# Performance work log

Hardware: AMD Instinct MI355X
Metric: run time of the kernel (lower is better)

The kernel has to match this reference:

```python
import jax, jax.numpy as jnp
import numpy as np

EPS = 1e-6

def _layernorm(x, g, b):
    m = jnp.mean(x, axis=-1, keepdims=True)
    v = jnp.var(x, axis=-1, keepdims=True)
    return (x - m) / jnp.sqrt(v + EPS) * g + b

def setup_inputs() -> dict:
    key = jax.random.key(0)
    ks = jax.random.split(key, 12)
    B, L, D, H = 2, 1024, 1024, 16
    s = 0.02  # weight init scale
    return {
        "query": jax.random.normal(ks[0], (B, L, D), jnp.float32),
        "pos_bias": jax.random.normal(ks[1], (H, L, L), jnp.float32) * 0.1,
        "postag_bias": jax.random.normal(ks[2], (B, H, L, L), jnp.float32) * 0.1,
        "lex_mask": jax.random.normal(ks[3], (B, L), jnp.float32) * 0.1,
        "mask": jax.random.randint(ks[4], (B, L), 0, 2).astype(jnp.int32),
        "Wq": jax.random.normal(ks[5], (D, D), jnp.float32) * s,
        "bq": jnp.zeros((D,), jnp.float32),
        "Wk": jax.random.normal(ks[6], (D, D), jnp.float32) * s,
        "bk": jnp.zeros((D,), jnp.float32),
        "Wv": jax.random.normal(ks[7], (D, D), jnp.float32) * s,
        "bv": jnp.zeros((D,), jnp.float32),
        "Wo": jax.random.normal(ks[8], (D, D), jnp.float32) * s,
        "bo": jnp.zeros((D,), jnp.float32),
        "gamma": jnp.ones((D,), jnp.float32),
        "beta": jnp.zeros((D,), jnp.float32),
    }

def reference(query, pos_bias, postag_bias, lex_mask, mask,
              Wq, bq, Wk, bk, Wv, bv, Wo, bo, gamma, beta):
    B, L, D = query.shape
    H = pos_bias.shape[0]
    dk = D // H
    scale = jnp.asarray(dk ** 0.5, query.dtype)

    residual = query
    context = query              # context=None path: set BEFORE pre-LN norm
    qn = _layernorm(query, gamma, beta)  # pre_ln=True applies only to query

    Q = (qn @ Wq.T + bq).reshape(B, L, H, dk)       # bqhd
    K = (context @ Wk.T + bk).reshape(B, L, H, dk)  # bkhd
    V = (context @ Wv.T + bv).reshape(B, L, H, dk)

    # (B,H,L,S) logits with all additive bias terms
    logits = jnp.einsum('bqhd,bkhd->bhqk', Q, K) / scale
    logits = logits + pos_bias[None]               # rel-pos bias (H,L,S)
    logits = logits + postag_bias                  # POS-tag bias (B,H,L,S)
    logits = logits + lex_mask[:, None, None, :]   # additive lexical mask
    logits = jnp.where(mask[:, None, None, :] == 0, -jnp.inf, logits)

    attn = jax.nn.softmax(logits, axis=-1)         # dropout inactive (eval)
    out = jnp.einsum('bhqk,bkhd->bqhd', attn, V).reshape(B, L, D)
    out = out @ Wo.T + bo
    out = out + residual
    return out, attn
```

## Files before the change

kernel.cpp:

```cpp
#include <hip/hip_runtime.h>
#include <hip/hip_bf16.h>
#include <math.h>

constexpr int B = 2, L = 1024, D = 1024, H = 16, DK = 64;
constexpr int M = B * L;
constexpr int DD = D * D;

typedef __attribute__((ext_vector_type(8))) short bf16x8;
typedef __attribute__((ext_vector_type(4))) float f32x4;

__device__ inline unsigned short f2bf(float f) {
    __hip_bfloat16 h = __float2bfloat16(f);
    return __builtin_bit_cast(unsigned short, h);
}

__device__ inline void glds16(const void* g, void* l) {
    __builtin_amdgcn_global_load_lds((const __attribute__((address_space(1))) void*)g,
                                     (__attribute__((address_space(3))) void*)l,
                                     16, 0, 0);
}

__global__ __launch_bounds__(256) void ln2_kernel(const float* __restrict__ x,
                                                  const float* __restrict__ gamma,
                                                  const float* __restrict__ beta,
                                                  unsigned short* __restrict__ qn16,
                                                  unsigned short* __restrict__ q16) {
    int row = blockIdx.x;
    int t = threadIdx.x;
    const float4 v = ((const float4*)(x + (size_t)row * D))[t];
    float s  = v.x + v.y + v.z + v.w;
    float sq = v.x*v.x + v.y*v.y + v.z*v.z + v.w*v.w;
    #pragma unroll
    for (int m = 32; m >= 1; m >>= 1) {
        s  += __shfl_xor(s, m, 64);
        sq += __shfl_xor(sq, m, 64);
    }
    __shared__ float rs[4], rq[4];
    int wid = t >> 6;
    if ((t & 63) == 0) { rs[wid] = s; rq[wid] = sq; }
    __syncthreads();
    s  = rs[0] + rs[1] + rs[2] + rs[3];
    sq = rq[0] + rq[1] + rq[2] + rq[3];
    float mean = s * (1.0f / D);
    float var  = sq * (1.0f / D) - mean * mean;
    float rstd = rsqrtf(var + 1e-6f);
    float4 g  = ((const float4*)gamma)[t];
    float4 bb = ((const float4*)beta)[t];
    ushort4 on, oq;
    on.x = f2bf((v.x - mean) * rstd * g.x + bb.x);
    on.y = f2bf((v.y - mean) * rstd * g.y + bb.y);
    on.z = f2bf((v.z - mean) * rstd * g.z + bb.z);
    on.w = f2bf((v.w - mean) * rstd * g.w + bb.w);
    oq.x = f2bf(v.x); oq.y = f2bf(v.y); oq.z = f2bf(v.z); oq.w = f2bf(v.w);
    ((ushort4*)(qn16 + (size_t)row * D))[t] = on;
    ((ushort4*)(q16  + (size_t)row * D))[t] = oq;
}

__global__ __launch_bounds__(256) void wconv_kernel(const float* __restrict__ Wq,
                                                    const float* __restrict__ Wk,
                                                    const float* __restrict__ Wv,
                                                    const float* __restrict__ Wo,
                                                    unsigned short* __restrict__ out) {
    const float* src = (blockIdx.y == 0) ? Wq : (blockIdx.y == 1) ? Wk
                       : (blockIdx.y == 2) ? Wv : Wo;
    size_t i = (size_t)blockIdx.x * 256 + threadIdx.x;
    float4 v = ((const float4*)src)[i];
    ushort4 o;
    o.x = f2bf(v.x); o.y = f2bf(v.y); o.z = f2bf(v.z); o.w = f2bf(v.w);
    ((ushort4*)(out + (size_t)blockIdx.y * DD))[i] = o;
}

__global__ __launch_bounds__(256) void lsm_kernel(const float* __restrict__ lex,
                                                  const int* __restrict__ mask,
                                                  float* __restrict__ lsm) {
    int i = blockIdx.x * 256 + threadIdx.x;
    lsm[i] = mask[i] ? lex[i] : -1e30f;
}

__global__ __launch_bounds__(256) void gemm_qkv(
        const unsigned short* __restrict__ qn16, const unsigned short* __restrict__ q16,
        const unsigned short* __restrict__ W,
        const float* __restrict__ bq, const float* __restrict__ bk,
        const float* __restrict__ bv,
        unsigned short* __restrict__ Qm, unsigned short* __restrict__ Km,
        unsigned short* __restrict__ Vm) {
    __shared__ __align__(16) unsigned short As[128 * 64];
    __shared__ __align__(16) unsigned short Ws[128 * 64];
    int t = threadIdx.x, lane = t & 63, w = t >> 6;
    int quad = lane >> 4, l15 = lane & 15;
    int nt = blockIdx.x;
    int bm = blockIdx.y * 128;
    const unsigned short* A = (nt < 8) ? qn16 : q16;
    const float* bias = (nt < 8) ? bq : ((nt < 16) ? bk : bv);
    unsigned short* Cout = (nt < 8) ? Qm : ((nt < 16) ? Km : Vm);
    int bn_local = (nt & 7) * 128;
    int wm = (w >> 1) * 64, wn = (w & 1) * 64;
    f32x4 acc[4][4] = {};
    for (int k0 = 0; k0 < D; k0 += 64) {
        __syncthreads();
        const unsigned short* ap = A + (size_t)(bm + w * 32) * D + k0;
        const unsigned short* wp = W + (size_t)(nt * 128 + w * 32) * D + k0;
        #pragma unroll
        for (int i = 0; i < 4; i++) {
            int c = i * 64 + lane;
            int r = c >> 3, g = (c & 7) ^ (r & 7);
            glds16(ap + (size_t)r * D + g * 8, &As[w * 2048 + i * 512]);
            glds16(wp + (size_t)r * D + g * 8, &Ws[w * 2048 + i * 512]);
        }
        __syncthreads();
        #pragma unroll
        for (int k2 = 0; k2 < 2; k2++) {
            bf16x8 av[4], bw[4];
            #pragma unroll
            for (int i = 0; i < 4; i++) {
                int r = wm + i * 16 + l15;
                av[i] = *(const bf16x8*)&As[r * 64 + (((quad + 4 * k2) ^ (r & 7)) * 8)];
            }
            #pragma unroll
            for (int j = 0; j < 4; j++) {
                int r = wn + j * 16 + l15;
                bw[j] = *(const bf16x8*)&Ws[r * 64 + (((quad + 4 * k2) ^ (r & 7)) * 8)];
            }
            #pragma unroll
            for (int i = 0; i < 4; i++)
                #pragma unroll
                for (int j = 0; j < 4; j++)
                    acc[i][j] = __builtin_amdgcn_mfma_f32_16x16x32_bf16(av[i], bw[j], acc[i][j], 0, 0, 0);
        }
    }
    #pragma unroll
    for (int j = 0; j < 4; j++) {
        int col = bn_local + wn + j * 16 + l15;
        float bcol = bias[col];
        #pragma unroll
        for (int i = 0; i < 4; i++)
            #pragma unroll
            for (int rg = 0; rg < 4; rg++) {
                int row = bm + wm + i * 16 + quad * 4 + rg;
                Cout[(size_t)row * D + col] = f2bf(acc[i][j][rg] + bcol);
            }
    }
}

__global__ __launch_bounds__(256) void vtrans_kernel(const unsigned short* __restrict__ Vm,
                                                     unsigned short* __restrict__ Vt) {
    __shared__ unsigned short sb[128 * 66];
    int t = threadIdx.x;
    int z = blockIdx.y;
    int b = z >> 4, h = z & 15;
    int s0 = blockIdx.x * 128;
    size_t base = (size_t)b * L * D + (size_t)h * 64;
    #pragma unroll
    for (int i = 0; i < 4; i++) {
        int idx = t + 256 * i;
        int r = idx >> 3, c8 = idx & 7;
        uint4 vv = *(const uint4*)&Vm[base + (size_t)(s0 + r) * D + c8 * 8];
        unsigned int* sp = (unsigned int*)&sb[r * 66 + c8 * 8];
        sp[0] = vv.x; sp[1] = vv.y; sp[2] = vv.z; sp[3] = vv.w;
    }
    __syncthreads();
    #pragma unroll
    for (int i = 0; i < 4; i++) {
        int idx = t + 256 * i;
        int d = idx >> 4, sc = idx & 15;
        unsigned short tmp[8];
        #pragma unroll
        for (int j = 0; j < 8; j++) tmp[j] = sb[(sc * 8 + j) * 66 + d];
        *(uint4*)&Vt[((size_t)z * 64 + d) * L + s0 + sc * 8] = *(uint4*)tmp;
    }
}

__global__ __launch_bounds__(256, 4) void attn_pv_kernel(
        const unsigned short* __restrict__ Qm, const unsigned short* __restrict__ Km,
        const unsigned short* __restrict__ Vt,
        const float* __restrict__ pos_bias, const float* __restrict__ postag,
        const float* __restrict__ lsm, float* __restrict__ attn_out,
        unsigned short* __restrict__ ctx16) {
    __shared__ __align__(16) unsigned short q_sh[16][72];
    __shared__ __align__(16) unsigned short kv_sh[128 * 64];
    __shared__ __align__(16) unsigned short p_sh[16][136];
    __shared__ float lsm_sh[1024];
    __shared__ float redA[16][4], redB[16][4];

    int t = threadIdx.x, lane = t & 63, w = t >> 6;
    int quad = lane >> 4, l15 = lane & 15;
    int qt = blockIdx.x & 63;
    int bh = blockIdx.x >> 6;
    int b = bh >> 4, h = bh & 15;
    int q0 = qt * 16;
    int q = q0 + l15;
    size_t base = (size_t)b * L * D + (size_t)h * DK;

    if (t < 128) {
        int r = t >> 3, c8 = t & 7;
        *(uint4*)&q_sh[r][c8 * 8] = *(const uint4*)&Qm[base + (size_t)(q0 + r) * D + c8 * 8];
    }
    ((float4*)lsm_sh)[t] = ((const float4*)(lsm + b * L))[t];
    __syncthreads();
    bf16x8 qb0 = *(const bf16x8*)&q_sh[l15][quad * 8];
    bf16x8 qb1 = *(const bf16x8*)&q_sh[l15][32 + quad * 8];

    const float* pbp = pos_bias + ((size_t)h * L + q) * L;
    const float* ptp = postag + ((size_t)bh * L + q) * L;

    f32x4 acc[16] = {};
    for (int st = 0; st < 8; st++) {
        __syncthreads();
        const unsigned short* kp = Km + base + (size_t)(st * 128 + w * 32) * D;
        #pragma unroll
        for (int i = 0; i < 4; i++) {
            int c = i * 64 + lane;
            int r = c >> 3, g = (c & 7) ^ (r & 7);
            glds16(kp + (size_t)r * D + g * 8, &kv_sh[w * 2048 + i * 512]);
        }
        int s_u0 = st * 128 + w * 16 + quad * 4;
        int s_u1 = s_u0 + 64;
        float4 pb0 = *(const float4*)(pbp + s_u0);
        float4 pt0 = *(const float4*)(ptp + s_u0);
        float4 pb1 = *(const float4*)(pbp + s_u1);
        float4 pt1 = *(const float4*)(ptp + s_u1);
        __syncthreads();
        #pragma unroll
        for (int u = 0; u < 2; u++) {
            int r = (u * 4 + w) * 16 + l15;
            bf16x8 ka0 = *(const bf16x8*)&kv_sh[r * 64 + ((quad ^ (r & 7)) * 8)];
            bf16x8 ka1 = *(const bf16x8*)&kv_sh[r * 64 + (((quad + 4) ^ (r & 7)) * 8)];
            int ti = 2 * st + u;
            acc[ti] = __builtin_amdgcn_mfma_f32_16x16x32_bf16(ka0, qb0, acc[ti], 0, 0, 0);
            acc[ti] = __builtin_amdgcn_mfma_f32_16x16x32_bf16(ka1, qb1, acc[ti], 0, 0, 0);
        }
        {
            int ti = 2 * st;
            float4 l0 = *(const float4*)&lsm_sh[s_u0];
            acc[ti][0] = acc[ti][0] * 0.125f + (pb0.x + pt0.x + l0.x);
            acc[ti][1] = acc[ti][1] * 0.125f + (pb0.y + pt0.y + l0.y);
            acc[ti][2] = acc[ti][2] * 0.125f + (pb0.z + pt0.z + l0.z);
            acc[ti][3] = acc[ti][3] * 0.125f + (pb0.w + pt0.w + l0.w);
            ti = 2 * st + 1;
            float4 l1 = *(const float4*)&lsm_sh[s_u1];
            acc[ti][0] = acc[ti][0] * 0.125f + (pb1.x + pt1.x + l1.x);
            acc[ti][1] = acc[ti][1] * 0.125f + (pb1.y + pt1.y + l1.y);
            acc[ti][2] = acc[ti][2] * 0.125f + (pb1.z + pt1.z + l1.z);
            acc[ti][3] = acc[ti][3] * 0.125f + (pb1.w + pt1.w + l1.w);
        }
    }
    float mx = -1e30f;
    #pragma unroll
    for (int ti = 0; ti < 16; ti++)
        #pragma unroll
        for (int rg = 0; rg < 4; rg++) mx = fmaxf(mx, acc[ti][rg]);
    mx = fmaxf(mx, __shfl_xor(mx, 16, 64));
    mx = fmaxf(mx, __shfl_xor(mx, 32, 64));
    if (quad == 0) redA[l15][w] = mx;
    __syncthreads();
    mx = fmaxf(fmaxf(redA[l15][0], redA[l15][1]), fmaxf(redA[l15][2], redA[l15][3]));
    float sum = 0.f;
    #pragma unroll
    for (int ti = 0; ti < 16; ti++)
        #pragma unroll
        for (int rg = 0; rg < 4; rg++) {
            float e = __expf(acc[ti][rg] - mx);
            acc[ti][rg] = e;
            sum += e;
        }
    sum += __shfl_xor(sum, 16, 64);
    sum += __shfl_xor(sum, 32, 64);
    if (quad == 0) redB[l15][w] = sum;
    __syncthreads();
    float inv = 1.0f / (redB[l15][0] + redB[l15][1] + redB[l15][2] + redB[l15][3]);
    #pragma unroll
    for (int ti = 0; ti < 16; ti++) {
        int s0 = (ti >> 1) * 128 + (ti & 1) * 64 + w * 16 + quad * 4;
        float4 o;
        o.x = acc[ti][0] * inv; o.y = acc[ti][1] * inv;
        o.z = acc[ti][2] * inv; o.w = acc[ti][3] * inv;
        acc[ti][0] = o.x; acc[ti][1] = o.y; acc[ti][2] = o.z; acc[ti][3] = o.w;
        *(float4*)&attn_out[((size_t)bh * L + q) * L + s0] = o;
    }
    f32x4 cacc = {};
    const unsigned short* vp = Vt + (size_t)bh * 64 * L;
    for (int st = 0; st < 8; st++) {
        __syncthreads();
        #pragma unroll
        for (int i = 0; i < 4; i++) {
            int r = w * 16 + i * 4 + (lane >> 4);
            int g = (lane & 15) ^ (r & 7);
            glds16(vp + (size_t)r * L + st * 128 + g * 8, &kv_sh[w * 2048 + i * 512]);
        }
        #pragma unroll
        for (int u = 0; u < 2; u++) {
            f32x4 p = acc[2 * st + u];
            ushort4 pu;
            pu.x = f2bf(p[0]); pu.y = f2bf(p[1]); pu.z = f2bf(p[2]); pu.w = f2bf(p[3]);
            *(ushort4*)&p_sh[l15][u * 64 + w * 16 + quad * 4] = pu;
        }
        __syncthreads();
        int rv = w * 16 + l15;
        #pragma unroll
        for (int kk = 0; kk < 4; kk++) {
            bf16x8 vf = *(const bf16x8*)&kv_sh[rv * 128 + (((kk * 4 + quad) ^ (rv & 7)) * 8)];
            bf16x8 pf = *(const bf16x8*)&p_sh[l15][kk * 32 + quad * 8];
            cacc = __builtin_amdgcn_mfma_f32_16x16x32_bf16(pf, vf, cacc, 0, 0, 0);
        }
    }
    size_t cbase = ((size_t)b * L + q0) * D + (size_t)h * 64 + w * 16 + l15;
    #pragma unroll
    for (int rg = 0; rg < 4; rg++)
        ctx16[cbase + (size_t)(quad * 4 + rg) * D] = f2bf(cacc[rg]);
}

__global__ __launch_bounds__(256) void gemm_out(
        const unsigned short* __restrict__ A, const unsigned short* __restrict__ W,
        const float* __restrict__ bias, const float* __restrict__ res,
        float* __restrict__ C) {
    __shared__ __align__(16) unsigned short As[64 * 64];
    __shared__ __align__(16) unsigned short Ws[64 * 64];
    int t = threadIdx.x, lane = t & 63, w = t >> 6;
    int quad = lane >> 4, l15 = lane & 15;
    int bm = blockIdx.x * 64, bn = blockIdx.y * 64;
    int wm = (w >> 1) * 32, wn = (w & 1) * 32;
    f32x4 acc[2][2] = {};
    for (int k0 = 0; k0 < D; k0 += 64) {
        __syncthreads();
        const unsigned short* ap = A + (size_t)(bm + w * 16) * D + k0;
        const unsigned short* wp = W + (size_t)(bn + w * 16) * D + k0;
        #pragma unroll
        for (int i = 0; i < 2; i++) {
            int c = i * 64 + lane;
            int r = c >> 3, g = (c & 7) ^ (r & 7);
            glds16(ap + (size_t)r * D + g * 8, &As[w * 1024 + i * 512]);
            glds16(wp + (size_t)r * D + g * 8, &Ws[w * 1024 + i * 512]);
        }
        __syncthreads();
        #pragma unroll
        for (int k2 = 0; k2 < 2; k2++) {
            bf16x8 av[2], bw[2];
            #pragma unroll
            for (int i = 0; i < 2; i++) {
                int r = wm + i * 16 + l15;
                av[i] = *(const bf16x8*)&As[r * 64 + (((quad + 4 * k2) ^ (r & 7)) * 8)];
            }
            #pragma unroll
            for (int j = 0; j < 2; j++) {
                int r = wn + j * 16 + l15;
                bw[j] = *(const bf16x8*)&Ws[r * 64 + (((quad + 4 * k2) ^ (r & 7)) * 8)];
            }
            #pragma unroll
            for (int i = 0; i < 2; i++)
                #pragma unroll
                for (int j = 0; j < 2; j++)
                    acc[i][j] = __builtin_amdgcn_mfma_f32_16x16x32_bf16(av[i], bw[j], acc[i][j], 0, 0, 0);
        }
    }
    #pragma unroll
    for (int j = 0; j < 2; j++) {
        int col = bn + wn + j * 16 + l15;
        float bcol = bias[col];
        #pragma unroll
        for (int i = 0; i < 2; i++)
            #pragma unroll
            for (int rg = 0; rg < 4; rg++) {
                int row = bm + wm + i * 16 + quad * 4 + rg;
                C[(size_t)row * D + col] = acc[i][j][rg] + bcol + res[(size_t)row * D + col];
            }
    }
}

extern "C" void kernel_launch(void* const* d_in, const int* in_sizes, int n_in,
                              void* d_out, int out_size, void* d_ws, size_t ws_size,
                              hipStream_t stream) {
    (void)in_sizes; (void)n_in; (void)out_size; (void)ws_size;
    const float* query  = (const float*)d_in[0];
    const float* pos_b  = (const float*)d_in[1];
    const float* postag = (const float*)d_in[2];
    const float* lex    = (const float*)d_in[3];
    const int*   mask   = (const int*)d_in[4];
    const float* Wq = (const float*)d_in[5];
    const float* bq = (const float*)d_in[6];
    const float* Wk = (const float*)d_in[7];
    const float* bk = (const float*)d_in[8];
    const float* Wv = (const float*)d_in[9];
    const float* bv = (const float*)d_in[10];
    const float* Wo = (const float*)d_in[11];
    const float* bo = (const float*)d_in[12];
    const float* gamma = (const float*)d_in[13];
    const float* beta  = (const float*)d_in[14];

    float* out  = (float*)d_out;
    float* attn = out + (size_t)B * L * D;

    unsigned short* ws16 = (unsigned short*)d_ws;
    const size_t NE = (size_t)M * D;
    unsigned short* qn16  = ws16;
    unsigned short* q16   = ws16 + NE;
    unsigned short* W16   = ws16 + 2 * NE;
    unsigned short* Qm16  = W16 + 4 * (size_t)DD;
    unsigned short* Km16  = Qm16 + NE;
    unsigned short* Vm16  = Km16 + NE;
    unsigned short* Vt16  = Vm16 + NE;
    unsigned short* ctx16 = Vt16 + NE;
    float* lsm = (float*)(ctx16 + NE);

    ln2_kernel<<<M, 256, 0, stream>>>(query, gamma, beta, qn16, q16);
    wconv_kernel<<<dim3(DD / 1024, 4), 256, 0, stream>>>(Wq, Wk, Wv, Wo, W16);
    lsm_kernel<<<M / 256, 256, 0, stream>>>(lex, mask, lsm);
    gemm_qkv<<<dim3(24, 16), 256, 0, stream>>>(qn16, q16, W16, bq, bk, bv,
                                               Qm16, Km16, Vm16);
    vtrans_kernel<<<dim3(8, 32), 256, 0, stream>>>(Vm16, Vt16);
    attn_pv_kernel<<<B * H * (L / 16), 256, 0, stream>>>(Qm16, Km16, Vt16,
                                                         pos_b, postag, lsm,
                                                         attn, ctx16);
    gemm_out<<<dim3(32, 16), 256, 0, stream>>>(ctx16, W16 + 3 * (size_t)DD, bo, query, out);
}
```

Before: 408.1 us.

## Load K/V fragments directly to registers and double-buffer P in attention kernel

The attention kernel no longer stages K and V tiles through LDS. Each lane loads its MFMA operand fragments straight from global memory, which removes two block barriers per step in the QK^T loop. In the PV loop, V fragments are prefetched one step ahead in registers and the P tile is double-buffered, so only one barrier per step remains. The separate lsm kernel is folded into the layernorm kernel, and occupancy is lowered to 3 blocks to make room for the extra registers. The trade-off is that fragment global loads are less coalesced and register pressure is higher.

```diff
diff --git a/kernel.cpp b/kernel.cpp
--- a/kernel.cpp
+++ b/kernel.cpp
@@ -23,10 +23,14 @@
 __global__ __launch_bounds__(256) void ln2_kernel(const float* __restrict__ x,
                                                   const float* __restrict__ gamma,
                                                   const float* __restrict__ beta,
+                                                  const float* __restrict__ lex,
+                                                  const int* __restrict__ mask,
                                                   unsigned short* __restrict__ qn16,
-                                                  unsigned short* __restrict__ q16) {
+                                                  unsigned short* __restrict__ q16,
+                                                  float* __restrict__ lsmout) {
     int row = blockIdx.x;
     int t = threadIdx.x;
+    if (t == 0) lsmout[row] = mask[row] ? lex[row] : -1e30f;
     const float4 v = ((const float4*)(x + (size_t)row * D))[t];
     float s  = v.x + v.y + v.z + v.w;
     float sq = v.x*v.x + v.y*v.y + v.z*v.z + v.w*v.w;
@@ -68,13 +72,6 @@
     ushort4 o;
     o.x = f2bf(v.x); o.y = f2bf(v.y); o.z = f2bf(v.z); o.w = f2bf(v.w);
     ((ushort4*)(out + (size_t)blockIdx.y * DD))[i] = o;
-}
-
-__global__ __launch_bounds__(256) void lsm_kernel(const float* __restrict__ lex,
-                                                  const int* __restrict__ mask,
-                                                  float* __restrict__ lsm) {
-    int i = blockIdx.x * 256 + threadIdx.x;
-    lsm[i] = mask[i] ? lex[i] : -1e30f;
 }
 
 __global__ __launch_bounds__(256) void gemm_qkv(
@@ -170,15 +167,14 @@
     }
 }
 
-__global__ __launch_bounds__(256, 4) void attn_pv_kernel(
+__global__ __launch_bounds__(256, 3) void attn_pv_kernel(
         const unsigned short* __restrict__ Qm, const unsigned short* __restrict__ Km,
         const unsigned short* __restrict__ Vt,
         const float* __restrict__ pos_bias, const float* __restrict__ postag,
         const float* __restrict__ lsm, float* __restrict__ attn_out,
         unsigned short* __restrict__ ctx16) {
     __shared__ __align__(16) unsigned short q_sh[16][72];
-    __shared__ __align__(16) unsigned short kv_sh[128 * 64];
-    __shared__ __align__(16) unsigned short p_sh[16][136];
+    __shared__ __align__(16) unsigned short p_sh[2][16][136];
     __shared__ float lsm_sh[1024];
     __shared__ float redA[16][4], redB[16][4];
 
@@ -202,47 +198,38 @@
 
     const float* pbp = pos_bias + ((size_t)h * L + q) * L;
     const float* ptp = postag + ((size_t)bh * L + q) * L;
+    const unsigned short* kp0 = Km + base + (size_t)((w) * 16 + l15) * D + quad * 8;
+    const unsigned short* kp1 = Km + base + (size_t)((4 + w) * 16 + l15) * D + quad * 8;
 
     f32x4 acc[16] = {};
+    #pragma unroll
     for (int st = 0; st < 8; st++) {
-        __syncthreads();
-        const unsigned short* kp = Km + base + (size_t)(st * 128 + w * 32) * D;
-        #pragma unroll
-        for (int i = 0; i < 4; i++) {
-            int c = i * 64 + lane;
-            int r = c >> 3, g = (c & 7) ^ (r & 7);
-            glds16(kp + (size_t)r * D + g * 8, &kv_sh[w * 2048 + i * 512]);
-        }
+        size_t ko = (size_t)st * 128 * D;
+        bf16x8 ka00 = *(const bf16x8*)(kp0 + ko);
+        bf16x8 ka01 = *(const bf16x8*)(kp0 + ko + 32);
+        bf16x8 ka10 = *(const bf16x8*)(kp1 + ko);
+        bf16x8 ka11 = *(const bf16x8*)(kp1 + ko + 32);
         int s_u0 = st * 128 + w * 16 + quad * 4;
         int s_u1 = s_u0 + 64;
         float4 pb0 = *(const float4*)(pbp + s_u0);
         float4 pt0 = *(const float4*)(ptp + s_u0);
         float4 pb1 = *(const float4*)(pbp + s_u1);
         float4 pt1 = *(const float4*)(ptp + s_u1);
-        __syncthreads();
-        #pragma unroll
-        for (int u = 0; u < 2; u++) {
-            int r = (u * 4 + w) * 16 + l15;
-            bf16x8 ka0 = *(const bf16x8*)&kv_sh[r * 64 + ((quad ^ (r & 7)) * 8)];
-            bf16x8 ka1 = *(const bf16x8*)&kv_sh[r * 64 + (((quad + 4) ^ (r & 7)) * 8)];
-            int ti = 2 * st + u;
-            acc[ti] = __builtin_amdgcn_mfma_f32_16x16x32_bf16(ka0, qb0, acc[ti], 0, 0, 0);
-            acc[ti] = __builtin_amdgcn_mfma_f32_16x16x32_bf16(ka1, qb1, acc[ti], 0, 0, 0);
-        }
-        {
-            int ti = 2 * st;
-            float4 l0 = *(const float4*)&lsm_sh[s_u0];
-            acc[ti][0] = acc[ti][0] * 0.125f + (pb0.x + pt0.x + l0.x);
-            acc[ti][1] = acc[ti][1] * 0.125f + (pb0.y + pt0.y + l0.y);
-            acc[ti][2] = acc[ti][2] * 0.125f + (pb0.z + pt0.z + l0.z);
-            acc[ti][3] = acc[ti][3] * 0.125f + (pb0.w + pt0.w + l0.w);
-            ti = 2 * st + 1;
-            float4 l1 = *(const float4*)&lsm_sh[s_u1];
-            acc[ti][0] = acc[ti][0] * 0.125f + (pb1.x + pt1.x + l1.x);
-            acc[ti][1] = acc[ti][1] * 0.125f + (pb1.y + pt1.y + l1.y);
-            acc[ti][2] = acc[ti][2] * 0.125f + (pb1.z + pt1.z + l1.z);
-            acc[ti][3] = acc[ti][3] * 0.125f + (pb1.w + pt1.w + l1.w);
-        }
+        float4 l0 = *(const float4*)&lsm_sh[s_u0];
+        float4 l1 = *(const float4*)&lsm_sh[s_u1];
+        int ti0 = 2 * st, ti1 = 2 * st + 1;
+        acc[ti0] = __builtin_amdgcn_mfma_f32_16x16x32_bf16(ka00, qb0, acc[ti0], 0, 0, 0);
+        acc[ti0] = __builtin_amdgcn_mfma_f32_16x16x32_bf16(ka01, qb1, acc[ti0], 0, 0, 0);
+        acc[ti1] = __builtin_amdgcn_mfma_f32_16x16x32_bf16(ka10, qb0, acc[ti1], 0, 0, 0);
+        acc[ti1] = __builtin_amdgcn_mfma_f32_16x16x32_bf16(ka11, qb1, acc[ti1], 0, 0, 0);
+        acc[ti0][0] = acc[ti0][0] * 0.125f + (pb0.x + pt0.x + l0.x);
+        acc[ti0][1] = acc[ti0][1] * 0.125f + (pb0.y + pt0.y + l0.y);
+        acc[ti0][2] = acc[ti0][2] * 0.125f + (pb0.z + pt0.z + l0.z);
+        acc[ti0][3] = acc[ti0][3] * 0.125f + (pb0.w + pt0.w + l0.w);
+        acc[ti1][0] = acc[ti1][0] * 0.125f + (pb1.x + pt1.x + l1.x);
+        acc[ti1][1] = acc[ti1][1] * 0.125f + (pb1.y + pt1.y + l1.y);
+        acc[ti1][2] = acc[ti1][2] * 0.125f + (pb1.z + pt1.z + l1.z);
+        acc[ti1][3] = acc[ti1][3] * 0.125f + (pb1.w + pt1.w + l1.w);
     }
     float mx = -1e30f;
     #pragma unroll
@@ -277,30 +264,39 @@
         acc[ti][0] = o.x; acc[ti][1] = o.y; acc[ti][2] = o.z; acc[ti][3] = o.w;
         *(float4*)&attn_out[((size_t)bh * L + q) * L + s0] = o;
     }
+    const unsigned short* vpl = Vt + ((size_t)bh * 64 + w * 16 + l15) * L + quad * 8;
     f32x4 cacc = {};
-    const unsigned short* vp = Vt + (size_t)bh * 64 * L;
+    bf16x8 vcur[4];
+    #pragma unroll
+    for (int kk = 0; kk < 4; kk++)
+        vcur[kk] = *(const bf16x8*)(vpl + kk * 32);
+    #pragma unroll
     for (int st = 0; st < 8; st++) {
-        __syncthreads();
-        #pragma unroll
-        for (int i = 0; i < 4; i++) {
-            int r = w * 16 + i * 4 + (lane >> 4);
-            int g = (lane & 15) ^ (r & 7);
-            glds16(vp + (size_t)r * L + st * 128 + g * 8, &kv_sh[w * 2048 + i * 512]);
-        }
         #pragma unroll
         for (int u = 0; u < 2; u++) {
             f32x4 p = acc[2 * st + u];
             ushort4 pu;
             pu.x = f2bf(p[0]); pu.y = f2bf(p[1]); pu.z = f2bf(p[2]); pu.w = f2bf(p[3]);
-            *(ushort4*)&p_sh[l15][u * 64 + w * 16 + quad * 4] = pu;
-        }
-        __syncthreads();
-        int rv = w * 16 + l15;
+            *(ushort4*)&p_sh[st & 1][l15][u * 64 + w * 16 + quad * 4] = pu;
+        }
+        bf16x8 vnext[4];
+        if (st < 7) {
+            #pragma unroll
+            for (int kk = 0; kk < 4; kk++)
+                vnext[kk] = *(const bf16x8*)(vpl + (st + 1) * 128 + kk * 32);
+        }
+        asm volatile("s_waitcnt lgkmcnt(0)" ::: "memory");
+        __builtin_amdgcn_sched_barrier(0);
+        __builtin_amdgcn_s_barrier();
+        __builtin_amdgcn_sched_barrier(0);
         #pragma unroll
         for (int kk = 0; kk < 4; kk++) {
-            bf16x8 vf = *(const bf16x8*)&kv_sh[rv * 128 + (((kk * 4 + quad) ^ (rv & 7)) * 8)];
-            bf16x8 pf = *(const bf16x8*)&p_sh[l15][kk * 32 + quad * 8];
-            cacc = __builtin_amdgcn_mfma_f32_16x16x32_bf16(pf, vf, cacc, 0, 0, 0);
+            bf16x8 pf = *(const bf16x8*)&p_sh[st & 1][l15][kk * 32 + quad * 8];
+            cacc = __builtin_amdgcn_mfma_f32_16x16x32_bf16(pf, vcur[kk], cacc, 0, 0, 0);
+        }
+        if (st < 7) {
+            #pragma unroll
+            for (int kk = 0; kk < 4; kk++) vcur[kk] = vnext[kk];
         }
     }
     size_t cbase = ((size_t)b * L + q0) * D + (size_t)h * 64 + w * 16 + l15;
@@ -401,9 +397,8 @@
     unsigned short* ctx16 = Vt16 + NE;
     float* lsm = (float*)(ctx16 + NE);
 
-    ln2_kernel<<<M, 256, 0, stream>>>(query, gamma, beta, qn16, q16);
+    ln2_kernel<<<M, 256, 0, stream>>>(query, gamma, beta, lex, mask, qn16, q16, lsm);
     wconv_kernel<<<dim3(DD / 1024, 4), 256, 0, stream>>>(Wq, Wk, Wv, Wo, W16);
-    lsm_kernel<<<M / 256, 256, 0, stream>>>(lex, mask, lsm);
     gemm_qkv<<<dim3(24, 16), 256, 0, stream>>>(qn16, q16, W16, bq, bk, bv,
                                                Qm16, Km16, Vm16);
     vtrans_kernel<<<dim3(8, 32), 256, 0, stream>>>(Vm16, Vt16);
```

New measurement: 432.1 us. +5.9%, slower.
